# Optimization experiments

Hardware: AMD Instinct MI355X
Metric: run time of the kernel (lower is better)

The kernel has to match this reference:

```python
import jax, jax.numpy as jnp
import numpy as np

EMBED_DIM = 1024
NUM_HEADS = 16
HEAD_DIM = EMBED_DIM // NUM_HEADS


def setup_inputs() -> dict:
    key = jax.random.key(0)
    k_x, k_qkv, k_w, k_b = jax.random.split(key, 4)
    B, N, C = 2, 2048, EMBED_DIM
    scale = 1.0 / np.sqrt(C)
    x = jax.random.normal(k_x, (B, N, C), dtype=jnp.float32)
    # nn.Linear(embed_dim, 3*embed_dim, bias=False): weight [3C, C]
    w_qkv = jax.random.normal(k_qkv, (3 * C, C), dtype=jnp.float32) * scale
    # nn.Linear(embed_dim, embed_dim): weight [C, C], bias [C]
    w_out = jax.random.normal(k_w, (C, C), dtype=jnp.float32) * scale
    b_out = jax.random.normal(k_b, (C,), dtype=jnp.float32) * scale
    return {"x": x, "w_qkv": w_qkv, "w_out": w_out, "b_out": b_out}


def reference(x, w_qkv, w_out, b_out):
    B, N, C = x.shape
    H, D = NUM_HEADS, HEAD_DIM
    # qkv projection: [B,N,3C] -> [3,B,H,N,D]
    qkv = jnp.einsum("bnc,fc->bnf", x, w_qkv)
    qkv = qkv.reshape(B, N, 3, H, D).transpose(2, 0, 3, 1, 4)
    q, k, v = qkv[0], qkv[1], qkv[2]
    # scaled dot-product attention (dropout p=0 / eval mode -> identity)
    scores = jnp.einsum("bhnd,bhmd->bhnm", q, k) / np.sqrt(D).astype(x.dtype)
    attn = jax.nn.softmax(scores, axis=-1)
    out = jnp.einsum("bhnm,bhmd->bhnd", attn, v)
    out = out.transpose(0, 2, 1, 3).reshape(B, N, C)
    return jnp.einsum("bnc,oc->bno", out, w_out) + b_out
```

## Files before the change

### kernel.cpp

```cpp
#include <hip/hip_runtime.h>
#include <hip/hip_bf16.h>

typedef unsigned short u16;
typedef __attribute__((ext_vector_type(4))) float f32x4;
typedef __attribute__((ext_vector_type(8))) short bf16x8;

#define MFMA16(a, b, c) __builtin_amdgcn_mfma_f32_16x16x32_bf16(a, b, c, 0, 0, 0)

__device__ __forceinline__ u16 f2bf(float f) {
    union { float f; unsigned u; } v;
    v.f = f;
    unsigned r = v.u + 0x7FFFu + ((v.u >> 16) & 1u);
    return (u16)(r >> 16);
}

__device__ __forceinline__ int4 pack8(const float4 a, const float4 b) {
    int4 r;
    r.x = (int)((unsigned)f2bf(a.x) | ((unsigned)f2bf(a.y) << 16));
    r.y = (int)((unsigned)f2bf(a.z) | ((unsigned)f2bf(a.w) << 16));
    r.z = (int)((unsigned)f2bf(b.x) | ((unsigned)f2bf(b.y) << 16));
    r.w = (int)((unsigned)f2bf(b.z) | ((unsigned)f2bf(b.w) << 16));
    return r;
}

__device__ __forceinline__ unsigned pk2(float a, float b) {
    __hip_bfloat162 t = __float22bfloat162_rn(make_float2(a, b));
    union { __hip_bfloat162 h; unsigned u; } c;
    c.h = t;
    return c.u;
}

__device__ __forceinline__ void gload_lds16(const u16* g, u16* l) {
    __builtin_amdgcn_global_load_lds(
        (const __attribute__((address_space(1))) void*)g,
        (__attribute__((address_space(3))) void*)l, 16, 0, 0);
}

__global__ __launch_bounds__(256) void cvt_kernel(
    const float* __restrict__ x, const float* __restrict__ wq,
    const float* __restrict__ wo, u16* __restrict__ outb)
{
    size_t i = ((size_t)blockIdx.x * 256 + threadIdx.x) * 8;
    const float* src;
    size_t off;
    if (i < 4194304)      { src = x;  off = i; }
    else if (i < 7340032) { src = wq; off = i - 4194304; }
    else                  { src = wo; off = i - 7340032; }
    float4 a = *(const float4*)(src + off);
    float4 b = *(const float4*)(src + off + 4);
    *(int4*)(outb + i) = pack8(a, b);
}

__global__ __launch_bounds__(256) void qkv_gemm_kernel(
    const u16* __restrict__ X, const u16* __restrict__ W,
    u16* __restrict__ qws, u16* __restrict__ kws, u16* __restrict__ vws)
{
    __shared__ __align__(16) u16 Ash[128 * 64];
    __shared__ __align__(16) u16 Bsh[128 * 64];
    const int bm = blockIdx.x, bn = blockIdx.y;
    const int tid = threadIdx.x;
    const int lane = tid & 63, wid = tid >> 6;
    const int wm = wid >> 1, wn = wid & 1;
    const int g = lane >> 4, lq = lane & 15;

    f32x4 acc[4][4];
#pragma unroll
    for (int i = 0; i < 4; i++)
#pragma unroll
        for (int j = 0; j < 4; j++) acc[i][j] = (f32x4){0.f, 0.f, 0.f, 0.f};

    const int lrow = lane >> 3;
    const int lchunk = (lane & 7) ^ lrow;
    const u16* Ab = X + (size_t)(bm * 128 + lrow) * 1024 + lchunk * 8;
    const u16* Bb = W + (size_t)(bn * 128 + lrow) * 1024 + lchunk * 8;

    for (int kt = 0; kt < 16; ++kt) {
#pragma unroll
        for (int i = 0; i < 4; i++) {
            int sub = i * 4 + wid;
            gload_lds16(Ab + (size_t)sub * 8192 + kt * 64, &Ash[sub * 512]);
            gload_lds16(Bb + (size_t)sub * 8192 + kt * 64, &Bsh[sub * 512]);
        }
        __syncthreads();
#pragma unroll
        for (int ka = 0; ka < 2; ka++) {
            bf16x8 af[4], bfr[4];
#pragma unroll
            for (int mt = 0; mt < 4; mt++) {
                int row = wm * 64 + mt * 16 + lq;
                af[mt] = *(const bf16x8*)&Ash[row * 64 + (((ka * 4 + g) ^ (row & 7)) << 3)];
            }
#pragma unroll
            for (int nt = 0; nt < 4; nt++) {
                int row = wn * 64 + nt * 16 + lq;
                bfr[nt] = *(const bf16x8*)&Bsh[row * 64 + (((ka * 4 + g) ^ (row & 7)) << 3)];
            }
#pragma unroll
            for (int mt = 0; mt < 4; mt++)
#pragma unroll
                for (int nt = 0; nt < 4; nt++)
                    acc[mt][nt] = MFMA16(af[mt], bfr[nt], acc[mt][nt]);
        }
        __syncthreads();
    }

#pragma unroll
    for (int mt = 0; mt < 4; mt++) {
#pragma unroll
        for (int nt = 0; nt < 4; nt++) {
            int f = bn * 128 + wn * 64 + nt * 16 + lq;
            int t = f >> 10, h = (f >> 6) & 15, d = f & 63;
            int mbase = bm * 128 + wm * 64 + mt * 16 + g * 4;
            int b = mbase >> 11, n0 = mbase & 2047;
            if (t == 0) {
#pragma unroll
                for (int r = 0; r < 4; r++)
                    qws[((size_t)(b * 16 + h) * 2048 + n0 + r) * 64 + d] =
                        f2bf(acc[mt][nt][r] * 0.18033688f);
            } else if (t == 1) {
#pragma unroll
                for (int r = 0; r < 4; r++)
                    kws[((size_t)(b * 16 + h) * 2048 + n0 + r) * 64 + d] =
                        f2bf(acc[mt][nt][r]);
            } else {
                ushort4 pk;
                pk.x = f2bf(acc[mt][nt][0]);
                pk.y = f2bf(acc[mt][nt][1]);
                pk.z = f2bf(acc[mt][nt][2]);
                pk.w = f2bf(acc[mt][nt][3]);
                *(ushort4*)&vws[((size_t)(b * 16 + h) * 64 + d) * 2048 + n0] = pk;
            }
        }
    }
}

__global__ __launch_bounds__(256) void attn_kernel(
    const u16* __restrict__ qws, const u16* __restrict__ kws,
    const u16* __restrict__ vws, u16* __restrict__ ows)
{
    __shared__ __align__(16) u16 Ksh[2][64 * 64];
    __shared__ __align__(16) u16 Vsh[2][64 * 64];
    __shared__ __align__(16) u16 Psh[4][32 * 64];
    const int bh = blockIdx.x, qt = blockIdx.y;
    const int b = bh >> 4, h = bh & 15;
    const int tid = threadIdx.x, wid = tid >> 6, lane = tid & 63;
    const int g = lane >> 4, lq = lane & 15;

    const u16* Qp = qws + ((size_t)bh * 2048 + qt * 128 + wid * 32) * 64;
    bf16x8 qf[2][2];
#pragma unroll
    for (int qa = 0; qa < 2; qa++) {
        qf[qa][0] = *(const bf16x8*)(Qp + (qa * 16 + lq) * 64 + g * 8);
        qf[qa][1] = *(const bf16x8*)(Qp + (qa * 16 + lq) * 64 + 32 + g * 8);
    }

    const int lrow = lane >> 3;
    const int lchunk = (lane & 7) ^ lrow;
    const u16* Kb = kws + (size_t)bh * 2048 * 64 + (size_t)lrow * 64 + lchunk * 8;
    const u16* Vb = vws + (size_t)bh * 64 * 2048 + (size_t)lrow * 2048 + lchunk * 8;

#define STAGE(KT, BUF)                                                        \
    {                                                                         \
        _Pragma("unroll")                                                     \
        for (int i = 0; i < 2; i++) {                                         \
            int sub = wid * 2 + i;                                            \
            gload_lds16(Kb + (size_t)((KT) * 64 + sub * 8) * 64,              \
                        &Ksh[BUF][sub * 512]);                                \
            gload_lds16(Vb + (size_t)(sub * 8) * 2048 + (KT) * 64,            \
                        &Vsh[BUF][sub * 512]);                                \
        }                                                                     \
    }

    bf16x8 onesB;
#pragma unroll
    for (int i = 0; i < 8; i++) onesB[i] = (short)0x3F80;

    f32x4 oacc[2][4];
#pragma unroll
    for (int qa = 0; qa < 2; qa++)
#pragma unroll
        for (int i = 0; i < 4; i++) oacc[qa][i] = (f32x4){0.f, 0.f, 0.f, 0.f};
    f32x4 lacc[2] = {(f32x4){0.f, 0.f, 0.f, 0.f}, (f32x4){0.f, 0.f, 0.f, 0.f}};

    STAGE(0, 0);

    for (int kt = 0; kt < 32; ++kt) {
        const int buf = kt & 1;
        STAGE((kt + 1) & 31, buf ^ 1);
        asm volatile("s_waitcnt vmcnt(4)" ::: "memory");
        __builtin_amdgcn_s_barrier();
        __builtin_amdgcn_sched_barrier(0);

#pragma unroll
        for (int qa = 0; qa < 2; qa++) {
            f32x4 s[4];
#pragma unroll
            for (int nt = 0; nt < 4; nt++) {
                int row = nt * 16 + lq;
                bf16x8 kb0 = *(const bf16x8*)&Ksh[buf][row * 64 + ((g ^ (row & 7)) << 3)];
                bf16x8 kb1 = *(const bf16x8*)&Ksh[buf][row * 64 + (((4 + g) ^ (row & 7)) << 3)];
                f32x4 z = (f32x4){0.f, 0.f, 0.f, 0.f};
                z = MFMA16(kb0, qf[qa][0], z);
                z = MFMA16(kb1, qf[qa][1], z);
                s[nt] = z;
            }
            int prow = qa * 16 + lq;
#pragma unroll
            for (int nt = 0; nt < 4; nt++) {
#pragma unroll
                for (int r = 0; r < 4; r++) s[nt][r] = __builtin_amdgcn_exp2f(s[nt][r]);
                uint2 pk;
                pk.x = pk2(s[nt][0], s[nt][1]);
                pk.y = pk2(s[nt][2], s[nt][3]);
                int c16 = nt * 2 + (g >> 1);
                *(uint2*)&Psh[wid][prow * 64 + (((c16 ^ (lq & 7)) << 3) | ((g & 1) << 2))] = pk;
            }
        }
        asm volatile("s_waitcnt lgkmcnt(0)" ::: "memory");
        __builtin_amdgcn_sched_barrier(0);

#pragma unroll
        for (int qa = 0; qa < 2; qa++) {
            int prow = qa * 16 + lq;
            bf16x8 pa0 = *(const bf16x8*)&Psh[wid][prow * 64 + ((g ^ (lq & 7)) << 3)];
            bf16x8 pa1 = *(const bf16x8*)&Psh[wid][prow * 64 + (((4 + g) ^ (lq & 7)) << 3)];
            lacc[qa] = MFMA16(pa0, onesB, lacc[qa]);
            lacc[qa] = MFMA16(pa1, onesB, lacc[qa]);
#pragma unroll
            for (int dt = 0; dt < 4; dt++) {
                int vrow = dt * 16 + lq;
                bf16x8 vb0 = *(const bf16x8*)&Vsh[buf][vrow * 64 + ((g ^ (vrow & 7)) << 3)];
                bf16x8 vb1 = *(const bf16x8*)&Vsh[buf][vrow * 64 + (((4 + g) ^ (vrow & 7)) << 3)];
                oacc[qa][dt] = MFMA16(pa0, vb0, oacc[qa][dt]);
                oacc[qa][dt] = MFMA16(pa1, vb1, oacc[qa][dt]);
            }
        }
        asm volatile("s_waitcnt lgkmcnt(0)" ::: "memory");
        __builtin_amdgcn_s_barrier();
    }
#undef STAGE

#pragma unroll
    for (int qa = 0; qa < 2; qa++)
#pragma unroll
        for (int dt = 0; dt < 4; dt++)
#pragma unroll
            for (int r = 0; r < 4; r++) {
                int n = qt * 128 + wid * 32 + qa * 16 + g * 4 + r;
                ows[((size_t)b * 2048 + n) * 1024 + h * 64 + dt * 16 + lq] =
                    f2bf(oacc[qa][dt][r] / lacc[qa][r]);
            }
}

__global__ __launch_bounds__(256) void out_gemm_kernel(
    const u16* __restrict__ A, const u16* __restrict__ W,
    const float* __restrict__ bias, float* __restrict__ Out)
{
    __shared__ __align__(16) u16 Ash[128 * 64];
    __shared__ __align__(16) u16 Bsh[128 * 64];
    const int bm = blockIdx.x, bn = blockIdx.y;
    const int tid = threadIdx.x;
    const int lane = tid & 63, wid = tid >> 6;
    const int wm = wid >> 1, wn = wid & 1;
    const int g = lane >> 4, lq = lane & 15;

    f32x4 acc[4][4];
#pragma unroll
    for (int i = 0; i < 4; i++)
#pragma unroll
        for (int j = 0; j < 4; j++) acc[i][j] = (f32x4){0.f, 0.f, 0.f, 0.f};

    const int lrow = lane >> 3;
    const int lchunk = (lane & 7) ^ lrow;
    const u16* Ab = A + (size_t)(bm * 128 + lrow) * 1024 + lchunk * 8;
    const u16* Bb = W + (size_t)(bn * 128 + lrow) * 1024 + lchunk * 8;

    for (int kt = 0; kt < 16; ++kt) {
#pragma unroll
        for (int i = 0; i < 4; i++) {
            int sub = i * 4 + wid;
            gload_lds16(Ab + (size_t)sub * 8192 + kt * 64, &Ash[sub * 512]);
            gload_lds16(Bb + (size_t)sub * 8192 + kt * 64, &Bsh[sub * 512]);
        }
        __syncthreads();
#pragma unroll
        for (int ka = 0; ka < 2; ka++) {
            bf16x8 af[4], bfr[4];
#pragma unroll
            for (int mt = 0; mt < 4; mt++) {
                int row = wm * 64 + mt * 16 + lq;
                af[mt] = *(const bf16x8*)&Ash[row * 64 + (((ka * 4 + g) ^ (row & 7)) << 3)];
            }
#pragma unroll
            for (int nt = 0; nt < 4; nt++) {
                int row = wn * 64 + nt * 16 + lq;
                bfr[nt] = *(const bf16x8*)&Bsh[row * 64 + (((ka * 4 + g) ^ (row & 7)) << 3)];
            }
#pragma unroll
            for (int mt = 0; mt < 4; mt++)
#pragma unroll
                for (int nt = 0; nt < 4; nt++)
                    acc[mt][nt] = MFMA16(af[mt], bfr[nt], acc[mt][nt]);
        }
        __syncthreads();
    }

#pragma unroll
    for (int mt = 0; mt < 4; mt++) {
#pragma unroll
        for (int nt = 0; nt < 4; nt++) {
            int ncol = bn * 128 + wn * 64 + nt * 16 + lq;
            float bv = bias[ncol];
            int mbase = bm * 128 + wm * 64 + mt * 16 + g * 4;
#pragma unroll
            for (int r = 0; r < 4; r++)
                Out[(size_t)(mbase + r) * 1024 + ncol] = acc[mt][nt][r] + bv;
        }
    }
}

extern "C" void kernel_launch(void* const* d_in, const int* in_sizes, int n_in,
                              void* d_out, int out_size, void* d_ws, size_t ws_size,
                              hipStream_t stream) {
    const float* x     = (const float*)d_in[0];
    const float* w_qkv = (const float*)d_in[1];
    const float* w_out = (const float*)d_in[2];
    const float* b_out = (const float*)d_in[3];
    float* out = (float*)d_out;

    u16* xb  = (u16*)d_ws;
    u16* wqb = xb + 4194304;
    u16* wob = wqb + 3145728;
    u16* qws = wob + 1048576;
    u16* kws = qws + 4194304;
    u16* vws = kws + 4194304;
    u16* ows = vws + 4194304;

    cvt_kernel<<<4096, 256, 0, stream>>>(x, w_qkv, w_out, xb);
    qkv_gemm_kernel<<<dim3(32, 24), 256, 0, stream>>>(xb, wqb, qws, kws, vws);
    attn_kernel<<<dim3(32, 16), 256, 0, stream>>>(qws, kws, vws, ows);
    out_gemm_kernel<<<dim3(32, 8), 256, 0, stream>>>(ows, wob, b_out, out);
}
```

Measured before the change: 127.5 us.

## Split attention KV range across blocks with larger Q tiles and combine kernel

Each attention block now handles 256 query rows (64 per wave) and only half of the key/value sequence, selected by a new grid z dimension. Partial unnormalized outputs and row sums are written in fp32 and merged by a new combine kernel. The larger Q tile reuses each staged K/V tile across more MFMAs, and the split keeps the block count the same. It also raises wave priority around the PV MFMAs and requests two blocks per CU. The cost is extra fp32 partial traffic, another kernel launch, and higher register pressure.

```diff
diff --git a/kernel.cpp b/kernel.cpp
--- a/kernel.cpp
+++ b/kernel.cpp
@@ -134,22 +134,22 @@
     }
 }
 
-__global__ __launch_bounds__(256) void attn_kernel(
+__global__ __launch_bounds__(256, 2) void attn_kernel(
     const u16* __restrict__ qws, const u16* __restrict__ kws,
-    const u16* __restrict__ vws, u16* __restrict__ ows)
+    const u16* __restrict__ vws, float* __restrict__ Opart,
+    float* __restrict__ lpart)
 {
     __shared__ __align__(16) u16 Ksh[2][64 * 64];
     __shared__ __align__(16) u16 Vsh[2][64 * 64];
-    __shared__ __align__(16) u16 Psh[4][32 * 64];
-    const int bh = blockIdx.x, qt = blockIdx.y;
-    const int b = bh >> 4, h = bh & 15;
+    __shared__ __align__(16) u16 Psh[4][64 * 64];
+    const int bh = blockIdx.x, qt = blockIdx.y, kvh = blockIdx.z;
     const int tid = threadIdx.x, wid = tid >> 6, lane = tid & 63;
     const int g = lane >> 4, lq = lane & 15;
 
-    const u16* Qp = qws + ((size_t)bh * 2048 + qt * 128 + wid * 32) * 64;
-    bf16x8 qf[2][2];
-#pragma unroll
-    for (int qa = 0; qa < 2; qa++) {
+    const u16* Qp = qws + ((size_t)bh * 2048 + qt * 256 + wid * 64) * 64;
+    bf16x8 qf[4][2];
+#pragma unroll
+    for (int qa = 0; qa < 4; qa++) {
         qf[qa][0] = *(const bf16x8*)(Qp + (qa * 16 + lq) * 64 + g * 8);
         qf[qa][1] = *(const bf16x8*)(Qp + (qa * 16 + lq) * 64 + 32 + g * 8);
     }
@@ -159,14 +159,14 @@
     const u16* Kb = kws + (size_t)bh * 2048 * 64 + (size_t)lrow * 64 + lchunk * 8;
     const u16* Vb = vws + (size_t)bh * 64 * 2048 + (size_t)lrow * 2048 + lchunk * 8;
 
-#define STAGE(KT, BUF)                                                        \
+#define STAGE(TG, BUF)                                                        \
     {                                                                         \
         _Pragma("unroll")                                                     \
         for (int i = 0; i < 2; i++) {                                         \
             int sub = wid * 2 + i;                                            \
-            gload_lds16(Kb + (size_t)((KT) * 64 + sub * 8) * 64,              \
+            gload_lds16(Kb + (size_t)((TG) * 64 + sub * 8) * 64,              \
                         &Ksh[BUF][sub * 512]);                                \
-            gload_lds16(Vb + (size_t)(sub * 8) * 2048 + (KT) * 64,            \
+            gload_lds16(Vb + (size_t)(sub * 8) * 2048 + (TG) * 64,            \
                         &Vsh[BUF][sub * 512]);                                \
         }                                                                     \
     }
@@ -175,81 +175,117 @@
 #pragma unroll
     for (int i = 0; i < 8; i++) onesB[i] = (short)0x3F80;
 
-    f32x4 oacc[2][4];
-#pragma unroll
-    for (int qa = 0; qa < 2; qa++)
+    f32x4 oacc[4][4];
+#pragma unroll
+    for (int qa = 0; qa < 4; qa++)
 #pragma unroll
         for (int i = 0; i < 4; i++) oacc[qa][i] = (f32x4){0.f, 0.f, 0.f, 0.f};
-    f32x4 lacc[2] = {(f32x4){0.f, 0.f, 0.f, 0.f}, (f32x4){0.f, 0.f, 0.f, 0.f}};
-
-    STAGE(0, 0);
-
-    for (int kt = 0; kt < 32; ++kt) {
-        const int buf = kt & 1;
-        STAGE((kt + 1) & 31, buf ^ 1);
+    f32x4 lacc[4];
+#pragma unroll
+    for (int qa = 0; qa < 4; qa++) lacc[qa] = (f32x4){0.f, 0.f, 0.f, 0.f};
+
+    const int tbase = kvh * 16;
+    STAGE(tbase, 0);
+
+    for (int t = 0; t < 16; ++t) {
+        const int buf = t & 1;
+        STAGE(tbase + ((t + 1) & 15), buf ^ 1);
         asm volatile("s_waitcnt vmcnt(4)" ::: "memory");
         __builtin_amdgcn_s_barrier();
         __builtin_amdgcn_sched_barrier(0);
 
 #pragma unroll
-        for (int qa = 0; qa < 2; qa++) {
-            f32x4 s[4];
-#pragma unroll
-            for (int nt = 0; nt < 4; nt++) {
-                int row = nt * 16 + lq;
-                bf16x8 kb0 = *(const bf16x8*)&Ksh[buf][row * 64 + ((g ^ (row & 7)) << 3)];
-                bf16x8 kb1 = *(const bf16x8*)&Ksh[buf][row * 64 + (((4 + g) ^ (row & 7)) << 3)];
+        for (int nt = 0; nt < 4; nt++) {
+            int row = nt * 16 + lq;
+            bf16x8 kb0 = *(const bf16x8*)&Ksh[buf][row * 64 + ((g ^ (row & 7)) << 3)];
+            bf16x8 kb1 = *(const bf16x8*)&Ksh[buf][row * 64 + (((4 + g) ^ (row & 7)) << 3)];
+            int c16 = nt * 2 + (g >> 1);
+#pragma unroll
+            for (int qa = 0; qa < 4; qa++) {
                 f32x4 z = (f32x4){0.f, 0.f, 0.f, 0.f};
                 z = MFMA16(kb0, qf[qa][0], z);
                 z = MFMA16(kb1, qf[qa][1], z);
-                s[nt] = z;
-            }
-            int prow = qa * 16 + lq;
-#pragma unroll
-            for (int nt = 0; nt < 4; nt++) {
-#pragma unroll
-                for (int r = 0; r < 4; r++) s[nt][r] = __builtin_amdgcn_exp2f(s[nt][r]);
+#pragma unroll
+                for (int r = 0; r < 4; r++) z[r] = __builtin_amdgcn_exp2f(z[r]);
                 uint2 pk;
-                pk.x = pk2(s[nt][0], s[nt][1]);
-                pk.y = pk2(s[nt][2], s[nt][3]);
-                int c16 = nt * 2 + (g >> 1);
+                pk.x = pk2(z[0], z[1]);
+                pk.y = pk2(z[2], z[3]);
+                int prow = qa * 16 + lq;
                 *(uint2*)&Psh[wid][prow * 64 + (((c16 ^ (lq & 7)) << 3) | ((g & 1) << 2))] = pk;
             }
         }
         asm volatile("s_waitcnt lgkmcnt(0)" ::: "memory");
         __builtin_amdgcn_sched_barrier(0);
 
-#pragma unroll
-        for (int qa = 0; qa < 2; qa++) {
-            int prow = qa * 16 + lq;
-            bf16x8 pa0 = *(const bf16x8*)&Psh[wid][prow * 64 + ((g ^ (lq & 7)) << 3)];
-            bf16x8 pa1 = *(const bf16x8*)&Psh[wid][prow * 64 + (((4 + g) ^ (lq & 7)) << 3)];
-            lacc[qa] = MFMA16(pa0, onesB, lacc[qa]);
-            lacc[qa] = MFMA16(pa1, onesB, lacc[qa]);
+        __builtin_amdgcn_s_setprio(1);
+#pragma unroll
+        for (int qp = 0; qp < 2; qp++) {
+            bf16x8 pa[2][2];
+#pragma unroll
+            for (int q2 = 0; q2 < 2; q2++) {
+                int prow = (qp * 2 + q2) * 16 + lq;
+                pa[q2][0] = *(const bf16x8*)&Psh[wid][prow * 64 + ((g ^ (lq & 7)) << 3)];
+                pa[q2][1] = *(const bf16x8*)&Psh[wid][prow * 64 + (((4 + g) ^ (lq & 7)) << 3)];
+                lacc[qp * 2 + q2] = MFMA16(pa[q2][0], onesB, lacc[qp * 2 + q2]);
+                lacc[qp * 2 + q2] = MFMA16(pa[q2][1], onesB, lacc[qp * 2 + q2]);
+            }
 #pragma unroll
             for (int dt = 0; dt < 4; dt++) {
                 int vrow = dt * 16 + lq;
                 bf16x8 vb0 = *(const bf16x8*)&Vsh[buf][vrow * 64 + ((g ^ (vrow & 7)) << 3)];
                 bf16x8 vb1 = *(const bf16x8*)&Vsh[buf][vrow * 64 + (((4 + g) ^ (vrow & 7)) << 3)];
-                oacc[qa][dt] = MFMA16(pa0, vb0, oacc[qa][dt]);
-                oacc[qa][dt] = MFMA16(pa1, vb1, oacc[qa][dt]);
-            }
-        }
+#pragma unroll
+                for (int q2 = 0; q2 < 2; q2++) {
+                    oacc[qp * 2 + q2][dt] = MFMA16(pa[q2][0], vb0, oacc[qp * 2 + q2][dt]);
+                    oacc[qp * 2 + q2][dt] = MFMA16(pa[q2][1], vb1, oacc[qp * 2 + q2][dt]);
+                }
+            }
+        }
+        __builtin_amdgcn_s_setprio(0);
         asm volatile("s_waitcnt lgkmcnt(0)" ::: "memory");
         __builtin_amdgcn_s_barrier();
     }
 #undef STAGE
 
-#pragma unroll
-    for (int qa = 0; qa < 2; qa++)
+    const int nbase = qt * 256 + wid * 64;
+#pragma unroll
+    for (int qa = 0; qa < 4; qa++) {
 #pragma unroll
         for (int dt = 0; dt < 4; dt++)
 #pragma unroll
             for (int r = 0; r < 4; r++) {
-                int n = qt * 128 + wid * 32 + qa * 16 + g * 4 + r;
-                ows[((size_t)b * 2048 + n) * 1024 + h * 64 + dt * 16 + lq] =
-                    f2bf(oacc[qa][dt][r] / lacc[qa][r]);
-            }
+                int n = nbase + qa * 16 + g * 4 + r;
+                Opart[(size_t)kvh * 4194304 + ((size_t)bh * 2048 + n) * 64 + dt * 16 + lq] =
+                    oacc[qa][dt][r];
+            }
+        if (lq == 0) {
+#pragma unroll
+            for (int r = 0; r < 4; r++)
+                lpart[kvh * 65536 + bh * 2048 + nbase + qa * 16 + g * 4 + r] =
+                    lacc[qa][r];
+        }
+    }
+}
+
+__global__ __launch_bounds__(256) void combine_kernel(
+    const float* __restrict__ Opart, const float* __restrict__ lpart,
+    u16* __restrict__ ows)
+{
+    int idx = blockIdx.x * 256 + threadIdx.x;
+    int d4 = (idx & 15) * 4;
+    int n  = (idx >> 4) & 2047;
+    int bh = idx >> 15;
+    size_t o = ((size_t)bh * 2048 + n) * 64 + d4;
+    float4 a = *(const float4*)(Opart + o);
+    float4 c = *(const float4*)(Opart + 4194304 + o);
+    float rl = 1.0f / (lpart[bh * 2048 + n] + lpart[65536 + bh * 2048 + n]);
+    ushort4 pk;
+    pk.x = f2bf((a.x + c.x) * rl);
+    pk.y = f2bf((a.y + c.y) * rl);
+    pk.z = f2bf((a.z + c.z) * rl);
+    pk.w = f2bf((a.w + c.w) * rl);
+    int b = bh >> 4, h = bh & 15;
+    *(ushort4*)&ows[((size_t)b * 2048 + n) * 1024 + h * 64 + d4] = pk;
 }
 
 __global__ __launch_bounds__(256) void out_gemm_kernel(
@@ -335,9 +371,12 @@
     u16* kws = qws + 4194304;
     u16* vws = kws + 4194304;
     u16* ows = vws + 4194304;
+    float* Opart = (float*)(ows + 4194304);
+    float* lpart = Opart + 8388608;
 
     cvt_kernel<<<4096, 256, 0, stream>>>(x, w_qkv, w_out, xb);
     qkv_gemm_kernel<<<dim3(32, 24), 256, 0, stream>>>(xb, wqb, qws, kws, vws);
-    attn_kernel<<<dim3(32, 16), 256, 0, stream>>>(qws, kws, vws, ows);
+    attn_kernel<<<dim3(32, 8, 2), 256, 0, stream>>>(qws, kws, vws, Opart, lpart);
+    combine_kernel<<<4096, 256, 0, stream>>>(Opart, lpart, ows);
     out_gemm_kernel<<<dim3(32, 8), 256, 0, stream>>>(ows, wob, b_out, out);
 }
```

Result: no change. 125.7 us (-1.4%).
